# Performance work log

Hardware: AMD Instinct MI355X
Metric: run time of the kernel (lower is better)

## Reference

```python
import jax, jax.numpy as jnp
import numpy as np

N_E = 512
E_DIM = 128
LEGACY = 0.2
B, T = 64, 1024


def setup_inputs() -> dict:
    key = jax.random.key(0)
    k1, k2 = jax.random.split(key, 2)
    key_soft = jax.random.normal(k1, (B, T, E_DIM), dtype=jnp.float32)
    emb_weight = jax.random.uniform(k2, (N_E + 1, E_DIM), dtype=jnp.float32,
                                    minval=-1.0 / N_E, maxval=1.0 / N_E)
    zero_ts_mask = jnp.zeros((B,), dtype=jnp.bool_)
    return {"key_soft": key_soft, "emb_weight": emb_weight, "zero_ts_mask": zero_ts_mask}


def _neighbor_indices(d, zero_ts_mask, n_e):
    # d: [B, T, n_e+1] (no grad needed; only used for int index selection)
    ind0 = jnp.clip(jnp.argmin(d[:, 0, :], axis=1), 0, n_e - 1)
    ind0 = jnp.where(zero_ts_mask, 0, ind0)

    def step(ind, d_t):  # ind: [B], d_t: [B, n_e+1]
        d_here = jnp.take_along_axis(d_t, ind[:, None], axis=1)[:, 0]
        ind_next = jnp.clip(ind + 1, 0, n_e - 1)
        d_next = jnp.take_along_axis(d_t, ind_next[:, None], axis=1)[:, 0]
        ind_new = jnp.where(d_here <= d_next, ind, ind_next)
        return ind_new, ind_new

    _, rest = jax.lax.scan(step, ind0, jnp.swapaxes(d[:, 1:, :], 0, 1))  # [T-1, B]
    return jnp.concatenate([ind0[None, :], rest], axis=0).T  # [B, T]


def reference(key_soft, emb_weight, zero_ts_mask):
    sg = jax.lax.stop_gradient
    n_e = emb_weight.shape[0] - 1
    b, t, e_dim = key_soft.shape

    # squared-distance matrix: [B, T, n_e+1]
    d = (jnp.sum(key_soft ** 2, axis=-1, keepdims=True)
         + jnp.sum(emb_weight ** 2, axis=1)
         - 2.0 * jnp.einsum('btd,nd->btn', key_soft, emb_weight))
    d_ng = sg(d)

    min_indices = jnp.argmin(d_ng, axis=-1)                 # [B, T] (over full n_e+1)
    enc = _neighbor_indices(d_ng, zero_ts_mask, n_e)        # [B, T]

    key_hard_here = emb_weight[enc]                                  # [B, T, D]
    key_hard_next = emb_weight[jnp.clip(enc + 1, 0, n_e - 1)]        # [B, T, D]
    key_min = emb_weight[min_indices]                                # [B, T, D]

    def vq_loss(kh):
        return (jnp.sum((sg(key_soft) - kh) ** 2, axis=-1)
                + jnp.sum((key_soft - sg(kh)) ** 2, axis=-1) * LEGACY)

    loss_here_base = vq_loss(key_hard_here)
    loss_next_base = vq_loss(key_hard_next)

    energy = (jnp.sum((sg(key_soft) - key_hard_next) ** 2, axis=-1)
              - jnp.sum((sg(key_soft) - key_hard_here) ** 2, axis=-1)
              + (jnp.sum((key_soft - sg(key_hard_next)) ** 2, axis=-1)
                 - jnp.sum((key_soft - sg(key_hard_here)) ** 2, axis=-1)) * LEGACY)

    change = (enc[:, 1:] - enc[:, :-1]) != 0
    same_hard_mask = jnp.where(change, 0.0, 1.0)
    energy_change = (energy[:, 1:] - energy[:, :-1]) * same_hard_mask
    loss_energy_descent = jnp.maximum(energy_change + 1e-06 / n_e,
                                      jnp.zeros_like(energy_change)).mean()
    energy_mean = energy.mean()

    loss_min_indices = vq_loss(key_min)
    loss_min_here = jnp.where(loss_min_indices < loss_here_base, loss_min_indices, 0.0)
    loss_min_next = jnp.where(loss_min_indices < loss_next_base, loss_min_indices, 0.0)

    loss_here = loss_here_base - loss_next_base - loss_min_here
    loss_next = loss_next_base - loss_here_base - loss_min_next

    key_hard = key_soft + sg(key_hard_here - key_soft)  # straight-through

    v = jnp.max(jnp.max(enc, axis=1) - jnp.min(enc, axis=1))
    return (key_hard, enc, v, loss_here, loss_next, energy_mean, loss_energy_descent)
```

## Files before the change

kernel.cpp:

```cpp
#include <hip/hip_runtime.h>
#include <cfloat>
#include <cstdint>

#define B_  64
#define T_  1024
#define D_  128
#define NE  512
#define P_  (B_*T_)

#define O_KH   0
#define O_ENC  (P_*D_)
#define O_V    (O_ENC + P_)
#define O_LH   (O_V + 1)
#define O_LN   (O_LH + P_)
#define O_EM   (O_LN + P_)
#define O_LED  (O_EM + 1)

typedef __attribute__((ext_vector_type(8))) short bf16x8;
typedef __attribute__((ext_vector_type(4))) float floatx4;
typedef unsigned long long u64;

__device__ __forceinline__ void pack8(const float4& a, const float4& b,
                                      uint4& h, uint4& l)
{
    float v[8] = {a.x,a.y,a.z,a.w,b.x,b.y,b.z,b.w};
    unsigned hw[4], lw[4];
    #pragma unroll
    for (int e = 0; e < 4; e++) {
        const unsigned ua = __float_as_uint(v[2*e]);
        const unsigned ub = __float_as_uint(v[2*e+1]);
        const float fa = __uint_as_float(ua & 0xffff0000u);
        const float fb = __uint_as_float(ub & 0xffff0000u);
        const unsigned da = __float_as_uint(v[2*e]   - fa);
        const unsigned db = __float_as_uint(v[2*e+1] - fb);
        hw[e] = (ub & 0xffff0000u) | (ua >> 16);
        lw[e] = (db & 0xffff0000u) | (da >> 16);
    }
    h = make_uint4(hw[0],hw[1],hw[2],hw[3]);
    l = make_uint4(lw[0],lw[1],lw[2],lw[3]);
}

__device__ __forceinline__ u64 shflx64(u64 v, int d)
{
    const int lo = __shfl_xor((int)(unsigned)(v & 0xffffffffULL), d);
    const int hi = __shfl_xor((int)(unsigned)(v >> 32), d);
    return ((u64)(unsigned)hi << 32) | (unsigned)lo;
}

__device__ __forceinline__ unsigned sortkey(float f)
{
    const unsigned b = __float_as_uint(f);
    return b ^ (unsigned)(((int)b >> 31) | (int)0x80000000);
}

__global__ __launch_bounds__(256) void kFG(const float* __restrict__ ks,
                                           const float* __restrict__ emb,
                                           unsigned short* __restrict__ ehi,
                                           unsigned short* __restrict__ elo,
                                           float* __restrict__ sq,
                                           unsigned short* __restrict__ khi,
                                           unsigned short* __restrict__ klo)
{
    if (blockIdx.x < 1024) {
        const int pt  = blockIdx.x;
        const int kh  = threadIdx.x >> 6;
        const int row = threadIdx.x & 63;
        const float4* src = (const float4*)(ks + ((size_t)pt*64 + row)*D_ + kh*32);
        #pragma unroll
        for (int g = 0; g < 4; g++) {
            uint4 h, l;
            pack8(src[2*g], src[2*g+1], h, l);
            const size_t o = ((size_t)(pt*16 + kh*4 + g)*64 + row)*8;
            *(uint4*)(khi + o) = h;
            *(uint4*)(klo + o) = l;
        }
    } else {
        const int t = (blockIdx.x - 1024) * 256 + threadIdx.x;
        const int n = t >> 2, kst = t & 3;
        const float4* src = (const float4*)(emb + (size_t)n * D_ + kst * 32);
        float ss = 0.f;
        #pragma unroll
        for (int g = 0; g < 4; g++) {
            const float4 a = src[2*g], b = src[2*g+1];
            ss += a.x*a.x + a.y*a.y + a.z*a.z + a.w*a.w
                + b.x*b.x + b.y*b.y + b.z*b.z + b.w*b.w;
            uint4 h, l;
            pack8(a, b, h, l);
            const int f = ((n >> 4) * 4 + kst) * 4 + g;
            *(uint4*)(ehi + (size_t)f*128 + (size_t)(n & 15)*8) = h;
            *(uint4*)(elo + (size_t)f*128 + (size_t)(n & 15)*8) = l;
        }
        ss += __shfl_xor(ss, 1);
        ss += __shfl_xor(ss, 2);
        if (kst == 0) sq[n] = ss;
    }
}

__global__ __launch_bounds__(256) void kA(const float* __restrict__ sq,
                                          const unsigned short* __restrict__ ehi,
                                          const unsigned short* __restrict__ elo,
                                          const unsigned short* __restrict__ khi,
                                          const unsigned short* __restrict__ klo,
                                          u64* __restrict__ bits,
                                          float* __restrict__ sfirst,
                                          float* __restrict__ slast,
                                          unsigned* __restrict__ mins,
                                          unsigned short* __restrict__ mini16)
{
    const int tid  = threadIdx.x;
    const int lane = tid & 63;
    const int wv   = tid >> 6;
    const int m    = lane & 15;
    const int q    = lane >> 4;
    const int pt   = blockIdx.x & 1023;
    const int p0   = pt * 64;
    const int ch   = (blockIdx.x >> 10) * 4 + wv;
    const int nb   = ch * 64;

    floatx4 acc[4][4];
    #pragma unroll
    for (int i = 0; i < 4; i++)
        #pragma unroll
        for (int j = 0; j < 4; j++)
            #pragma unroll
            for (int r = 0; r < 4; r++) acc[i][j][r] = 0.f;

    bf16x8 ah[4], al[4], bh0[4], bl0[4], bh1[4], bl1[4];

    auto loadA = [&](int kst) {
        #pragma unroll
        for (int i = 0; i < 4; i++) {
            const int off = (((ch*4 + i) * 4 + kst) * 4 + q) * 128 + m*8;
            ah[i] = *(const bf16x8*)(ehi + off);
            al[i] = *(const bf16x8*)(elo + off);
        }
    };
    auto loadB = [&](int kst, bf16x8* BH, bf16x8* BL) {
        #pragma unroll
        for (int j = 0; j < 4; j++) {
            const int off = ((pt*16 + kst*4 + q) * 64 + j*16 + m) * 8;
            BH[j] = *(const bf16x8*)(khi + off);
            BL[j] = *(const bf16x8*)(klo + off);
        }
    };
    auto mfma3 = [&](const bf16x8* BH, const bf16x8* BL) {
        #pragma unroll
        for (int i = 0; i < 4; i++)
            #pragma unroll
            for (int j = 0; j < 4; j++)
                acc[i][j] = __builtin_amdgcn_mfma_f32_16x16x32_bf16(ah[i], BH[j], acc[i][j], 0, 0, 0);
        #pragma unroll
        for (int i = 0; i < 4; i++)
            #pragma unroll
            for (int j = 0; j < 4; j++)
                acc[i][j] = __builtin_amdgcn_mfma_f32_16x16x32_bf16(ah[i], BL[j], acc[i][j], 0, 0, 0);
        #pragma unroll
        for (int i = 0; i < 4; i++)
            #pragma unroll
            for (int j = 0; j < 4; j++)
                acc[i][j] = __builtin_amdgcn_mfma_f32_16x16x32_bf16(al[i], BH[j], acc[i][j], 0, 0, 0);
    };

    loadB(0, bh0, bl0);
    loadA(0);
    loadB(1, bh1, bl1);
    mfma3(bh0, bl0);
    loadA(1);
    loadB(2, bh0, bl0);
    mfma3(bh1, bl1);
    loadA(2);
    loadB(3, bh1, bl1);
    mfma3(bh0, bl0);
    loadA(3);
    mfma3(bh1, bl1);

    float sa[4][4];
    #pragma unroll
    for (int i = 0; i < 4; i++) {
        const float4 s4 = *(const float4*)(sq + nb + i*16 + q*4);
        sa[i][0]=s4.x; sa[i][1]=s4.y; sa[i][2]=s4.z; sa[i][3]=s4.w;
    }
    #pragma unroll
    for (int j = 0; j < 4; j++) {
        float S[4][4];
        #pragma unroll
        for (int i = 0; i < 4; i++)
            #pragma unroll
            for (int r = 0; r < 4; r++)
                S[i][r] = fmaf(-2.f, acc[i][j][r], sa[i][r]);

        float nq[4], ni[4];
        #pragma unroll
        for (int i = 0; i < 4; i++) nq[i] = __shfl_down(S[i][0], 16);
        #pragma unroll
        for (int i = 0; i < 3; i++) ni[i] = __shfl(S[i+1][0], m);
        ni[3] = 0.f;

        u64 w = 0;
        #pragma unroll
        for (int i = 0; i < 4; i++) {
            #pragma unroll
            for (int r = 0; r < 3; r++)
                w |= (u64)(S[i][r] <= S[i][r+1]) << (16*i + 4*q + r);
            if (!(i == 3 && q == 3)) {
                const float nxt = (q < 3) ? nq[i] : ni[i];
                w |= (u64)(S[i][3] <= nxt) << (16*i + 4*q + 3);
            }
        }
        if (ch == 7 && q == 3) w |= 1ULL << 63;
        w |= shflx64(w, 16);
        w |= shflx64(w, 32);

        float mv = S[0][0]; int mi_ = nb + q*4;
        #pragma unroll
        for (int i = 0; i < 4; i++)
            #pragma unroll
            for (int r = 0; r < 4; r++) {
                if (i == 0 && r == 0) continue;
                const int nid = nb + 16*i + 4*q + r;
                if (S[i][r] < mv) { mv = S[i][r]; mi_ = nid; }
            }
        #pragma unroll
        for (int d = 16; d <= 32; d <<= 1) {
            const float v2 = __shfl_xor(mv, d);
            const int   i2 = __shfl_xor(mi_, d);
            if (v2 < mv || (v2 == mv && i2 < mi_)) { mv = v2; mi_ = i2; }
        }

        const size_t pg = (size_t)(p0 + j*16 + m);
        if (q == 0) {
            bits  [pg*8 + ch] = w;
            sfirst[pg*8 + ch] = S[0][0];
            mins  [pg*8 + ch] = sortkey(mv);
            mini16[pg*8 + ch] = (unsigned short)mi_;
        }
        if (q == 3) slast[pg*8 + ch] = S[3][3];
    }
}

struct KBwin { u64 W[8]; float F[8]; float L[8]; };

__global__ __launch_bounds__(64) void kB(const float* __restrict__ ks,
                                         const float* __restrict__ emb,
                                         const unsigned char* __restrict__ mask,
                                         const u64* __restrict__ bits,
                                         const float* __restrict__ sfirst,
                                         const float* __restrict__ slast,
                                         const unsigned* __restrict__ mins,
                                         const unsigned short* __restrict__ mini16,
                                         int* __restrict__ enci,
                                         float* __restrict__ out)
{
    const int b    = blockIdx.x;
    const int lane = threadIdx.x;
    const size_t p0 = (size_t)b * T_;

    const float2 e = ((const float2*)(emb + (size_t)512*D_))[lane];
    const float2 k = ((const float2*)(ks  + p0*D_))[lane];
    float s5 = e.x*(e.x - 2.f*k.x) + e.y*(e.y - 2.f*k.y);
    #pragma unroll
    for (int m = 32; m >= 1; m >>= 1) s5 += __shfl_xor(s5, m);

    u64 kk = ~0ULL;
    if (lane < 8)       kk = ((u64)mins[p0*8 + lane] << 32) | (u64)mini16[p0*8 + lane];
    else if (lane == 8) kk = ((u64)sortkey(s5) << 32) | 512ULL;
    #pragma unroll
    for (int d = 1; d <= 8; d <<= 1) {
        const u64 o = shflx64(kk, d);
        kk = (o < kk) ? o : kk;
    }
    const int mi = __shfl((int)(unsigned)(kk & 0xffffffffULL), 0);
    int cur = (mi < NE) ? mi : NE - 1;
    if (mask[b]) cur = 0;
    if (lane == 0) { enci[p0] = cur; out[O_ENC + p0] = (float)cur; }

    KBwin wa, wb;

    auto loadwin = [&](KBwin& d, int t0) {
        const int t = t0 + lane;
        if (t < T_) {
            const ulonglong2* bp = (const ulonglong2*)(bits + (p0 + t)*8);
            const ulonglong2 w01 = bp[0], w23 = bp[1], w45 = bp[2], w67 = bp[3];
            d.W[0]=w01.x; d.W[1]=w01.y; d.W[2]=w23.x; d.W[3]=w23.y;
            d.W[4]=w45.x; d.W[5]=w45.y; d.W[6]=w67.x; d.W[7]=w67.y;
            const float4* fp = (const float4*)(sfirst + (p0 + t)*8);
            const float4 f0 = fp[0], f1 = fp[1];
            d.F[0]=f0.x; d.F[1]=f0.y; d.F[2]=f0.z; d.F[3]=f0.w;
            d.F[4]=f1.x; d.F[5]=f1.y; d.F[6]=f1.z; d.F[7]=f1.w;
            const float4* lp = (const float4*)(slast + (p0 + t)*8);
            const float4 l0 = lp[0], l1 = lp[1];
            d.L[0]=l0.x; d.L[1]=l0.y; d.L[2]=l0.z; d.L[3]=l0.w;
            d.L[4]=l1.x; d.L[5]=l1.y; d.L[6]=l1.z; d.L[7]=l1.w;
        } else {
            #pragma unroll
            for (int c = 0; c < 8; c++) { d.W[c] = ~0ULL; d.F[c] = 1.f; d.L[c] = 0.f; }
        }
    };

    auto scanwin = [&](KBwin& d, int t0) {
        #pragma unroll
        for (int c = 0; c < 7; c++)
            d.W[c] |= (u64)(d.L[c] <= d.F[c+1]) << 63;

        const int w0   = cur >> 6;
        const int off0 = cur & 63;
        u64 a = d.W[0];
        #pragma unroll
        for (int c = 1; c < 8; c++) a = (w0 == c) ? d.W[c] : a;
        u64 bn = ~0ULL;
        #pragma unroll
        for (int c = 1; c < 8; c++) bn = (w0 == c-1) ? d.W[c] : bn;
        const u64 u = (off0 == 0) ? a : ((a >> off0) | (bn << (64 - off0)));

        const unsigned ulo = (unsigned)u;
        const unsigned uhi = (unsigned)(u >> 32);
        int doff = 0;
        int myenc = cur;
        #pragma unroll
        for (int j = 0; j < 64; j++) {
            const unsigned slo = (unsigned)__builtin_amdgcn_readlane((int)ulo, j);
            const unsigned shi = (unsigned)__builtin_amdgcn_readlane((int)uhi, j);
            const u64 word = ((u64)shi << 32) | slo;
            const int bit = (int)((word >> doff) & 1ULL);
            doff += 1 - bit;
            if (lane == j) myenc = cur + doff;
        }
        cur += doff;
        const int t = t0 + lane;
        if (t < T_) {
            enci[p0 + t] = myenc;
            out[O_ENC + p0 + t] = (float)myenc;
        }
    };

    loadwin(wa, 1);
    #pragma unroll 1
    for (int wp = 0; wp < 8; wp++) {
        const int t0a = 1 + wp*128;
        loadwin(wb, t0a + 64);
        scanwin(wa, t0a);
        if (wp < 7) loadwin(wa, t0a + 128);
        scanwin(wb, t0a + 64);
    }
}

__global__ __launch_bounds__(256) void kC(const float* __restrict__ ks,
                                          const float* __restrict__ emb,
                                          const int* __restrict__ enci,
                                          const unsigned* __restrict__ mins,
                                          const unsigned short* __restrict__ mini16,
                                          float* __restrict__ out,
                                          float* __restrict__ energy)
{
    const int lane = threadIdx.x & 63;
    const size_t p = (size_t)blockIdx.x * 4 + (threadIdx.x >> 6);
    const int q  = lane >> 4;
    const int qm = lane & 15;

    const int eh = enci[p];
    const int en = (eh + 1 < NE) ? eh + 1 : NE - 1;
    const int row = (q == 0) ? eh : ((q == 1) ? en : 512);

    const float4* ksp = (const float4*)(ks + p*D_);
    const float4 k1 = ksp[qm*2], k2 = ksp[qm*2 + 1];
    const float4* ep = (const float4*)(emb + (size_t)row*D_);
    const float4 e1 = ep[qm*2], e2 = ep[qm*2 + 1];

    float d;
    if (q == 3) {
        d = k1.x*k1.x + k1.y*k1.y + k1.z*k1.z + k1.w*k1.w
          + k2.x*k2.x + k2.y*k2.y + k2.z*k2.z + k2.w*k2.w;
    } else {
        d = e1.x*(e1.x - 2.f*k1.x) + e1.y*(e1.y - 2.f*k1.y)
          + e1.z*(e1.z - 2.f*k1.z) + e1.w*(e1.w - 2.f*k1.w)
          + e2.x*(e2.x - 2.f*k2.x) + e2.y*(e2.y - 2.f*k2.y)
          + e2.z*(e2.z - 2.f*k2.z) + e2.w*(e2.w - 2.f*k2.w);
    }
    #pragma unroll
    for (int s = 1; s <= 8; s <<= 1) d += __shfl_xor(d, s);

    const float ph  = __shfl(d, 0);
    const float pn  = __shfl(d, 16);
    const float p5  = __shfl(d, 32);
    const float sqk = __shfl(d, 48);

    u64 kk = ~0ULL;
    if (lane < 8)       kk = ((u64)mins[p*8 + lane] << 32) | (u64)mini16[p*8 + lane];
    else if (lane == 8) kk = ((u64)sortkey(p5) << 32) | 512ULL;
    #pragma unroll
    for (int s = 1; s <= 8; s <<= 1) {
        const u64 o = shflx64(kk, s);
        kk = (o < kk) ? o : kk;
    }
    const int mi = __shfl((int)(unsigned)(kk & 0xffffffffULL), 0);

    float pm;
    if (mi == eh)      pm = ph;
    else if (mi == en) pm = pn;
    else if (mi == 512) pm = p5;
    else {
        const float4* mp = (const float4*)(emb + (size_t)mi*D_);
        const float4 m1 = mp[qm*2], m2 = mp[qm*2 + 1];
        float dm = m1.x*(m1.x - 2.f*k1.x) + m1.y*(m1.y - 2.f*k1.y)
                 + m1.z*(m1.z - 2.f*k1.z) + m1.w*(m1.w - 2.f*k1.w)
                 + m2.x*(m2.x - 2.f*k2.x) + m2.y*(m2.y - 2.f*k2.y)
                 + m2.z*(m2.z - 2.f*k2.z) + m2.w*(m2.w - 2.f*k2.w);
        #pragma unroll
        for (int s = 1; s <= 8; s <<= 1) dm += __shfl_xor(dm, s);
        pm = __shfl(dm, 0);
    }

    if (q == 0) {
        float4 o1, o2;
        o1.x = k1.x + (e1.x - k1.x); o1.y = k1.y + (e1.y - k1.y);
        o1.z = k1.z + (e1.z - k1.z); o1.w = k1.w + (e1.w - k1.w);
        o2.x = k2.x + (e2.x - k2.x); o2.y = k2.y + (e2.y - k2.y);
        o2.z = k2.z + (e2.z - k2.z); o2.w = k2.w + (e2.w - k2.w);
        ((float4*)(out + p*D_))[qm*2]     = o1;
        ((float4*)(out + p*D_))[qm*2 + 1] = o2;
    }

    if (lane == 0) {
        const float lh = 1.2f * (sqk + ph);
        const float ln = 1.2f * (sqk + pn);
        const float lm = 1.2f * (sqk + pm);
        out[O_LH + p] = lh - ln - ((pm < ph) ? lm : 0.f);
        out[O_LN + p] = ln - lh - ((pm < pn) ? lm : 0.f);
        energy[p] = 1.2f * (pn - ph);
    }
}

__global__ __launch_bounds__(256) void kD1(const float* __restrict__ energy,
                                           const int* __restrict__ enci,
                                           double2* __restrict__ part)
{
    __shared__ double sA[256], sB[256];
    const int p = blockIdx.x * 256 + threadIdx.x;
    const float e = energy[p];
    double se = (double)e;
    double sl = 0.0;
    if ((p & (T_-1)) < T_-1) {
        const float ec = (enci[p+1] == enci[p]) ? (energy[p+1] - e) : 0.f;
        sl = (double)fmaxf(ec + (float)(1e-6/512.0), 0.f);
    }
    sA[threadIdx.x] = se; sB[threadIdx.x] = sl;
    __syncthreads();
    for (int s = 128; s >= 1; s >>= 1) {
        if (threadIdx.x < (unsigned)s) {
            sA[threadIdx.x] += sA[threadIdx.x+s];
            sB[threadIdx.x] += sB[threadIdx.x+s];
        }
        __syncthreads();
    }
    if (threadIdx.x == 0) { part[blockIdx.x] = make_double2(sA[0], sB[0]); }
}

__global__ __launch_bounds__(256) void kD2(const double2* __restrict__ part,
                                           const int* __restrict__ enci,
                                           float* __restrict__ out)
{
    __shared__ double sA[256], sB[256];
    const double2 pv = part[threadIdx.x];
    sA[threadIdx.x] = pv.x; sB[threadIdx.x] = pv.y;
    __syncthreads();
    for (int s = 128; s >= 1; s >>= 1) {
        if (threadIdx.x < (unsigned)s) {
            sA[threadIdx.x] += sA[threadIdx.x+s];
            sB[threadIdx.x] += sB[threadIdx.x+s];
        }
        __syncthreads();
    }
    if (threadIdx.x < 64) {
        int v = enci[(size_t)threadIdx.x*T_ + T_-1] - enci[(size_t)threadIdx.x*T_];
        #pragma unroll
        for (int m = 32; m >= 1; m >>= 1) {
            const int v2 = __shfl_xor(v, m);
            v = (v2 > v) ? v2 : v;
        }
        if (threadIdx.x == 0) {
            out[O_V]   = (float)v;
            out[O_EM]  = (float)(sA[0] / (double)P_);
            out[O_LED] = (float)(sB[0] / (double)(B_*(T_-1)));
        }
    }
}

extern "C" void kernel_launch(void* const* d_in, const int* in_sizes, int n_in,
                              void* d_out, int out_size, void* d_ws, size_t ws_size,
                              hipStream_t stream)
{
    const float* ks  = (const float*)d_in[0];
    const float* emb = (const float*)d_in[1];
    const unsigned char* mask = (const unsigned char*)d_in[2];

    float* out = (float*)d_out;
    char* w = (char*)d_ws;
    u64*      bits   = (u64*)     (w);
    float*    sfirst = (float*)   (w + (size_t) 4*1024*1024);
    float*    slast  = (float*)   (w + (size_t) 6*1024*1024);
    unsigned* mins   = (unsigned*)(w + (size_t) 8*1024*1024);
    unsigned short* mini16 = (unsigned short*)(w + (size_t)10*1024*1024);
    int*      enci   = (int*)     (w + (size_t)11*1024*1024);
    float*    energy = (float*)   (w + (size_t)11*1024*1024 + 256*1024);
    float*    sq     = (float*)   (w + (size_t)11*1024*1024 + 512*1024);
    double2*  part   = (double2*) (w + (size_t)11*1024*1024 + 516*1024);
    unsigned short* ehi = (unsigned short*)(w + (size_t)11*1024*1024 + 640*1024);
    unsigned short* elo = (unsigned short*)(w + (size_t)11*1024*1024 + 768*1024);
    unsigned short* khi = (unsigned short*)d_out;
    unsigned short* klo = (unsigned short*)((char*)d_out + (size_t)16*1024*1024);

    kFG<<<1032, 256, 0, stream>>>(ks, emb, ehi, elo, sq, khi, klo);
    kA <<<2048, 256, 0, stream>>>(sq, ehi, elo, khi, klo, bits, sfirst, slast, mins, mini16);
    kB <<<B_,   64,  0, stream>>>(ks, emb, mask, bits, sfirst, slast, mins, mini16, enci, out);
    kC <<<P_/4, 256, 0, stream>>>(ks, emb, enci, mins, mini16, out, energy);
    kD1<<<256,  256, 0, stream>>>(energy, enci, part);
    kD2<<<1,    256, 0, stream>>>(part, enci, out);
}
```

Baseline: 194.9 us.

## Fuse key_soft bf16 split-packing into distance GEMM kernel

The pre-pass that split key_soft into hi/lo bf16 tiles and wrote them to scratch is removed. The GEMM kernel now loads fp32 key_soft directly and packs it into hi/lo fragments in registers before the MFMAs, so the prep kernel only handles the small embedding table. This saves a 32MB write plus a 32MB reread, but every kA block repacks its activations redundantly: key_soft is read by 8 channel-group blocks per tile, and the double-buffered B fragments are replaced by a single fp32 staging buffer.

Result: no change. 197.8 us (+1.5%).

```diff
diff --git a/kernel.cpp b/kernel.cpp
--- a/kernel.cpp
+++ b/kernel.cpp
@@ -53,54 +53,35 @@
     return b ^ (unsigned)(((int)b >> 31) | (int)0x80000000);
 }
 
-__global__ __launch_bounds__(256) void kFG(const float* __restrict__ ks,
-                                           const float* __restrict__ emb,
+__global__ __launch_bounds__(256) void kFG(const float* __restrict__ emb,
                                            unsigned short* __restrict__ ehi,
                                            unsigned short* __restrict__ elo,
-                                           float* __restrict__ sq,
-                                           unsigned short* __restrict__ khi,
-                                           unsigned short* __restrict__ klo)
-{
-    if (blockIdx.x < 1024) {
-        const int pt  = blockIdx.x;
-        const int kh  = threadIdx.x >> 6;
-        const int row = threadIdx.x & 63;
-        const float4* src = (const float4*)(ks + ((size_t)pt*64 + row)*D_ + kh*32);
-        #pragma unroll
-        for (int g = 0; g < 4; g++) {
-            uint4 h, l;
-            pack8(src[2*g], src[2*g+1], h, l);
-            const size_t o = ((size_t)(pt*16 + kh*4 + g)*64 + row)*8;
-            *(uint4*)(khi + o) = h;
-            *(uint4*)(klo + o) = l;
-        }
-    } else {
-        const int t = (blockIdx.x - 1024) * 256 + threadIdx.x;
-        const int n = t >> 2, kst = t & 3;
-        const float4* src = (const float4*)(emb + (size_t)n * D_ + kst * 32);
-        float ss = 0.f;
-        #pragma unroll
-        for (int g = 0; g < 4; g++) {
-            const float4 a = src[2*g], b = src[2*g+1];
-            ss += a.x*a.x + a.y*a.y + a.z*a.z + a.w*a.w
-                + b.x*b.x + b.y*b.y + b.z*b.z + b.w*b.w;
-            uint4 h, l;
-            pack8(a, b, h, l);
-            const int f = ((n >> 4) * 4 + kst) * 4 + g;
-            *(uint4*)(ehi + (size_t)f*128 + (size_t)(n & 15)*8) = h;
-            *(uint4*)(elo + (size_t)f*128 + (size_t)(n & 15)*8) = l;
-        }
-        ss += __shfl_xor(ss, 1);
-        ss += __shfl_xor(ss, 2);
-        if (kst == 0) sq[n] = ss;
-    }
-}
-
-__global__ __launch_bounds__(256) void kA(const float* __restrict__ sq,
+                                           float* __restrict__ sq)
+{
+    const int t = blockIdx.x * 256 + threadIdx.x;
+    const int n = t >> 2, kst = t & 3;
+    const float4* src = (const float4*)(emb + (size_t)n * D_ + kst * 32);
+    float ss = 0.f;
+    #pragma unroll
+    for (int g = 0; g < 4; g++) {
+        const float4 a = src[2*g], b = src[2*g+1];
+        ss += a.x*a.x + a.y*a.y + a.z*a.z + a.w*a.w
+            + b.x*b.x + b.y*b.y + b.z*b.z + b.w*b.w;
+        uint4 h, l;
+        pack8(a, b, h, l);
+        const int f = ((n >> 4) * 4 + kst) * 4 + g;
+        *(uint4*)(ehi + (size_t)f*128 + (size_t)(n & 15)*8) = h;
+        *(uint4*)(elo + (size_t)f*128 + (size_t)(n & 15)*8) = l;
+    }
+    ss += __shfl_xor(ss, 1);
+    ss += __shfl_xor(ss, 2);
+    if (kst == 0) sq[n] = ss;
+}
+
+__global__ __launch_bounds__(256) void kA(const float* __restrict__ ks,
+                                          const float* __restrict__ sq,
                                           const unsigned short* __restrict__ ehi,
                                           const unsigned short* __restrict__ elo,
-                                          const unsigned short* __restrict__ khi,
-                                          const unsigned short* __restrict__ klo,
                                           u64* __restrict__ bits,
                                           float* __restrict__ sfirst,
                                           float* __restrict__ slast,
@@ -125,7 +106,8 @@
             #pragma unroll
             for (int r = 0; r < 4; r++) acc[i][j][r] = 0.f;
 
-    bf16x8 ah[4], al[4], bh0[4], bl0[4], bh1[4], bl1[4];
+    bf16x8 ah[4], al[4], bh[4], bl[4];
+    float4 F[8];
 
     auto loadA = [&](int kst) {
         #pragma unroll
@@ -135,44 +117,58 @@
             al[i] = *(const bf16x8*)(elo + off);
         }
     };
-    auto loadB = [&](int kst, bf16x8* BH, bf16x8* BL) {
+    auto issueB = [&](int kst) {
         #pragma unroll
         for (int j = 0; j < 4; j++) {
-            const int off = ((pt*16 + kst*4 + q) * 64 + j*16 + m) * 8;
-            BH[j] = *(const bf16x8*)(khi + off);
-            BL[j] = *(const bf16x8*)(klo + off);
+            const float4* src = (const float4*)(ks + (size_t)(p0 + j*16 + m)*D_
+                                                + kst*32 + q*8);
+            F[2*j]   = src[0];
+            F[2*j+1] = src[1];
         }
     };
-    auto mfma3 = [&](const bf16x8* BH, const bf16x8* BL) {
+    auto packB = [&]() {
+        #pragma unroll
+        for (int j = 0; j < 4; j++) {
+            uint4 h, l;
+            pack8(F[2*j], F[2*j+1], h, l);
+            bh[j] = *(const bf16x8*)&h;
+            bl[j] = *(const bf16x8*)&l;
+        }
+    };
+    auto mfma3 = [&]() {
         #pragma unroll
         for (int i = 0; i < 4; i++)
             #pragma unroll
             for (int j = 0; j < 4; j++)
-                acc[i][j] = __builtin_amdgcn_mfma_f32_16x16x32_bf16(ah[i], BH[j], acc[i][j], 0, 0, 0);
+                acc[i][j] = __builtin_amdgcn_mfma_f32_16x16x32_bf16(ah[i], bh[j], acc[i][j], 0, 0, 0);
         #pragma unroll
         for (int i = 0; i < 4; i++)
             #pragma unroll
             for (int j = 0; j < 4; j++)
-                acc[i][j] = __builtin_amdgcn_mfma_f32_16x16x32_bf16(ah[i], BL[j], acc[i][j], 0, 0, 0);
+                acc[i][j] = __builtin_amdgcn_mfma_f32_16x16x32_bf16(ah[i], bl[j], acc[i][j], 0, 0, 0);
         #pragma unroll
         for (int i = 0; i < 4; i++)
             #pragma unroll
             for (int j = 0; j < 4; j++)
-                acc[i][j] = __builtin_amdgcn_mfma_f32_16x16x32_bf16(al[i], BH[j], acc[i][j], 0, 0, 0);
+                acc[i][j] = __builtin_amdgcn_mfma_f32_16x16x32_bf16(al[i], bh[j], acc[i][j], 0, 0, 0);
     };
 
-    loadB(0, bh0, bl0);
+    issueB(0);
     loadA(0);
-    loadB(1, bh1, bl1);
-    mfma3(bh0, bl0);
+    packB();
+    issueB(1);
+    mfma3();
     loadA(1);
-    loadB(2, bh0, bl0);
-    mfma3(bh1, bl1);
+    packB();
+    issueB(2);
+    mfma3();
     loadA(2);
-    loadB(3, bh1, bl1);
-    mfma3(bh0, bl0);
+    packB();
+    issueB(3);
+    mfma3();
     loadA(3);
-    mfma3(bh1, bl1);
+    packB();
+    mfma3();
 
     float sa[4][4];
     #pragma unroll
@@ -506,11 +502,9 @@
     double2*  part   = (double2*) (w + (size_t)11*1024*1024 + 516*1024);
     unsigned short* ehi = (unsigned short*)(w + (size_t)11*1024*1024 + 640*1024);
     unsigned short* elo = (unsigned short*)(w + (size_t)11*1024*1024 + 768*1024);
-    unsigned short* khi = (unsigned short*)d_out;
-    unsigned short* klo = (unsigned short*)((char*)d_out + (size_t)16*1024*1024);
-
-    kFG<<<1032, 256, 0, stream>>>(ks, emb, ehi, elo, sq, khi, klo);
-    kA <<<2048, 256, 0, stream>>>(sq, ehi, elo, khi, klo, bits, sfirst, slast, mins, mini16);
+
+    kFG<<<8,    256, 0, stream>>>(emb, ehi, elo, sq);
+    kA <<<2048, 256, 0, stream>>>(ks, sq, ehi, elo, bits, sfirst, slast, mins, mini16);
     kB <<<B_,   64,  0, stream>>>(ks, emb, mask, bits, sfirst, slast, mins, mini16, enci, out);
     kC <<<P_/4, 256, 0, stream>>>(ks, emb, enci, mins, mini16, out, energy);
     kD1<<<256,  256, 0, stream>>>(energy, enci, part);
```
